# Optimization experiments

Measured on AMD Instinct MI355X. Metric: run time of the kernel, lower is better.

## Reference

```python
import jax, jax.numpy as jnp
import numpy as np

B, T, D, H = 2, 2048, 1024, 16
DK = D // H

def setup_inputs() -> dict:
    key = jax.random.key(0)
    ks = jax.random.split(key, 12)
    s = 1.0 / np.sqrt(D)
    inp = {
        'Q': jax.random.normal(ks[0], (B, T, D), jnp.float32),
        'K': jax.random.normal(ks[1], (B, T, D), jnp.float32),
        'V': jax.random.normal(ks[2], (B, T, D), jnp.float32),
        'mask': jnp.tril(jnp.ones((T, T), jnp.int32))[None, None],  # causal [1,1,T,T]
        'Wq_w': jax.random.normal(ks[3], (D, D), jnp.float32) * s,
        'Wq_b': jax.random.normal(ks[4], (D,), jnp.float32) * s,
        'Wk_w': jax.random.normal(ks[5], (D, D), jnp.float32) * s,
        'Wk_b': jax.random.normal(ks[6], (D,), jnp.float32) * s,
        'Wv_w': jax.random.normal(ks[7], (D, D), jnp.float32) * s,
        'Wv_b': jax.random.normal(ks[8], (D,), jnp.float32) * s,
        'Wo_w': jax.random.normal(ks[9], (D, D), jnp.float32) * s,
        'Wo_b': jax.random.normal(ks[10], (D,), jnp.float32) * s,
    }
    return inp

def reference(Q, K, V, mask, Wq_w, Wq_b, Wk_w, Wk_b, Wv_w, Wv_b, Wo_w, Wo_b):
    b, tq, c = Q.shape
    tk = K.shape[1]
    q = (Q @ Wq_w + Wq_b).reshape(b, tq, H, DK).transpose(0, 2, 1, 3)  # [B,H,Tq,dk]
    k = (K @ Wk_w + Wk_b).reshape(b, tk, H, DK).transpose(0, 2, 1, 3)
    v = (V @ Wv_w + Wv_b).reshape(b, tk, H, DK).transpose(0, 2, 1, 3)
    scores = jnp.einsum('bhqd,bhkd->bhqk', q, k) / jnp.sqrt(jnp.float32(DK))
    scores = jnp.where(mask == 0, jnp.float32(-1e9), scores)
    attn = jax.nn.softmax(scores, axis=-1)
    out = jnp.einsum('bhqk,bhkd->bhqd', attn, v)
    out = out.transpose(0, 2, 1, 3).reshape(b, tq, c)
    return out @ Wo_w + Wo_b
```

## Files before the change

### kernel.cpp

```cpp
#include <hip/hip_runtime.h>
#include <hip/hip_bf16.h>

#define NB 2
#define NT 2048
#define ND 1024
#define NH 16
#define NDK 64

typedef __attribute__((ext_vector_type(8))) short bf16x8;
typedef __attribute__((ext_vector_type(4))) float f32x4;

static __device__ __forceinline__ short f2bf(float f) {
  union { float f; unsigned u; } c; c.f = f;
  unsigned u = c.u;
  u += 0x7FFF + ((u >> 16) & 1);
  return (short)(u >> 16);
}

static __device__ __forceinline__ unsigned cvt_pk_bf16(float lo, float hi) {
  unsigned r;
  asm("v_cvt_pk_bf16_f32 %0, %1, %2" : "=v"(r) : "v"(lo), "v"(hi));
  return r;
}

static __device__ __forceinline__ void gload16(const void* g, void* l) {
  __builtin_amdgcn_global_load_lds((const __attribute__((address_space(1))) void*)g,
                                   (__attribute__((address_space(3))) void*)l, 16, 0, 0);
}

__global__ void cast3_kernel(const float* __restrict__ s0, const float* __restrict__ s1,
                             const float* __restrict__ s2,
                             short* __restrict__ t0, short* __restrict__ t1,
                             short* __restrict__ t2) {
  int z = blockIdx.x >> 11;
  int i = (blockIdx.x & 2047) * 256 + threadIdx.x;
  const float* src = z == 0 ? s0 : (z == 1 ? s1 : s2);
  short* dst       = z == 0 ? t0 : (z == 1 ? t1 : t2);
  const float4* s4 = (const float4*)src + (size_t)i * 2;
  float4 a = s4[0], b = s4[1];
  bf16x8 o;
  o[0] = f2bf(a.x); o[1] = f2bf(a.y); o[2] = f2bf(a.z); o[3] = f2bf(a.w);
  o[4] = f2bf(b.x); o[5] = f2bf(b.y); o[6] = f2bf(b.z); o[7] = f2bf(b.w);
  *((bf16x8*)dst + i) = o;
}

__global__ void wtrans_kernel(const float* __restrict__ W0, const float* __restrict__ W1,
                              const float* __restrict__ W2, const float* __restrict__ W3,
                              short* __restrict__ T0, short* __restrict__ T1,
                              short* __restrict__ T2, short* __restrict__ T3) {
  __shared__ float t[32][33];
  int z = blockIdx.z;
  const float* W = z == 0 ? W0 : (z == 1 ? W1 : (z == 2 ? W2 : W3));
  short* Wt      = z == 0 ? T0 : (z == 1 ? T1 : (z == 2 ? T2 : T3));
  int n0 = blockIdx.x * 32, k0 = blockIdx.y * 32;
  int tx = threadIdx.x, ty = threadIdx.y;
  for (int i = ty; i < 32; i += 8) t[i][tx] = W[(size_t)(k0 + i) * ND + n0 + tx];
  __syncthreads();
  for (int i = ty; i < 32; i += 8) Wt[(size_t)(n0 + i) * ND + k0 + tx] = f2bf(t[tx][i]);
}

template <int MODE, int BN>
__global__ __launch_bounds__(256, 2) void gemm_bt(
    const short* __restrict__ A0, const short* __restrict__ A1, const short* __restrict__ A2,
    const short* __restrict__ W0, const short* __restrict__ W1, const short* __restrict__ W2,
    const float* __restrict__ b0, const float* __restrict__ b1, const float* __restrict__ b2,
    void* o0, void* o1, void* o2)
{
  constexpr int K = ND;
  constexpr int NI = BN / 32;
  constexpr int NNB = ND / BN;
  constexpr int NZ = (MODE == 0) ? 3 : 1;
  constexpr int NWPX = NZ * 32 * NNB / 8;
  __shared__ short As[2][128 * 32];
  __shared__ short Bs[2][BN * 32];

  int d = blockIdx.x;
  int work = (d & 7) * NWPX + (d >> 3);
  int z = work / (32 * NNB);
  int rem = work % (32 * NNB);
  int m0 = (rem / NNB) * 128, n0 = (rem % NNB) * BN;

  const short* A    = z == 0 ? A0 : (z == 1 ? A1 : A2);
  const short* Wt   = z == 0 ? W0 : (z == 1 ? W1 : W2);
  const float* bias = z == 0 ? b0 : (z == 1 ? b1 : b2);
  void* out         = z == 0 ? o0 : (z == 1 ? o1 : o2);
  float scl = (MODE == 0 && z == 0) ? 0.18033688011112042f : 1.0f;

  int tid = threadIdx.x, wid = tid >> 6, lane = tid & 63;
  int wr = wid >> 1, wc = wid & 1;
  int r16 = lane & 15, l4 = lane >> 4;

  auto stage = [&](int buf, int kt) {
    int row = (lane >> 2);
    int c8 = (lane & 3) * 8;
    {
      int rbase = wid * 32;
      const short* ga = A + (size_t)(m0 + rbase + row) * K + kt * 32 + c8;
      gload16(ga,          &As[buf][rbase * 32]);
      gload16(ga + 16 * K, &As[buf][(rbase + 16) * 32]);
    }
    if constexpr (BN == 128) {
      int rbase = wid * 32;
      const short* gb = Wt + (size_t)(n0 + rbase + row) * K + kt * 32 + c8;
      gload16(gb,          &Bs[buf][rbase * 32]);
      gload16(gb + 16 * K, &Bs[buf][(rbase + 16) * 32]);
    } else {
      int rbase = wid * 16;
      const short* gb = Wt + (size_t)(n0 + rbase + row) * K + kt * 32 + c8;
      gload16(gb,          &Bs[buf][rbase * 32]);
    }
  };

  f32x4 acc[4][NI] = {};
  stage(0, 0);
  __syncthreads();

  for (int kt = 0; kt < K / 32; ++kt) {
    int cur = kt & 1;
    if (kt + 1 < K / 32) stage(cur ^ 1, kt + 1);
    bf16x8 af[4], bfv[NI];
    int kk = l4 * 8;
#pragma unroll
    for (int mi = 0; mi < 4; mi++)
      af[mi] = *(const bf16x8*)&As[cur][(wr * 64 + mi * 16 + r16) * 32 + kk];
#pragma unroll
    for (int ni = 0; ni < NI; ni++)
      bfv[ni] = *(const bf16x8*)&Bs[cur][(wc * (BN / 2) + ni * 16 + r16) * 32 + kk];
#pragma unroll
    for (int mi = 0; mi < 4; mi++)
#pragma unroll
      for (int ni = 0; ni < NI; ni++)
        acc[mi][ni] = __builtin_amdgcn_mfma_f32_16x16x32_bf16(af[mi], bfv[ni], acc[mi][ni], 0, 0, 0);
    __syncthreads();
  }

  int mb = m0 + wr * 64, nb = n0 + wc * (BN / 2);
#pragma unroll
  for (int mi = 0; mi < 4; mi++)
#pragma unroll
    for (int ni = 0; ni < NI; ni++) {
      int n = nb + ni * 16 + r16;
      float bv = bias[n];
      if constexpr (MODE == 0) {
        int h = n >> 6, dk = n & 63;
        if (z == 2) {
          int m0_ = mb + mi * 16 + l4 * 4;
          int bI = m0_ >> 11, t0 = m0_ & (NT - 1);
          int bh = bI * NH + h;
          short4 s4;
          s4.x = f2bf(acc[mi][ni][0] + bv);
          s4.y = f2bf(acc[mi][ni][1] + bv);
          s4.z = f2bf(acc[mi][ni][2] + bv);
          s4.w = f2bf(acc[mi][ni][3] + bv);
          *(short4*)&((short*)out)[(size_t)bh * 131072 + (dk >> 4) * 32768 +
                                   (t0 >> 3) * 128 + (dk & 15) * 8 + (t0 & 7)] = s4;
        } else if (z == 1) {
#pragma unroll
          for (int r = 0; r < 4; r++) {
            int m = mb + mi * 16 + l4 * 4 + r;
            int bI = m >> 11, t = m & (NT - 1);
            int bh = bI * NH + h;
            ((short*)out)[(size_t)bh * 131072 + (t >> 4) * 1024 + (dk >> 3) * 128 +
                          (t & 15) * 8 + (dk & 7)] = f2bf(acc[mi][ni][r] + bv);
          }
        } else {
#pragma unroll
          for (int r = 0; r < 4; r++) {
            int m = mb + mi * 16 + l4 * 4 + r;
            int bI = m >> 11, t = m & (NT - 1);
            ((short*)out)[((((size_t)bI * NH + h) * NT + t) << 6) + dk] = f2bf((acc[mi][ni][r] + bv) * scl);
          }
        }
      } else {
#pragma unroll
        for (int r = 0; r < 4; r++) {
          int m = mb + mi * 16 + l4 * 4 + r;
          ((float*)out)[(size_t)m * ND + n] = acc[mi][ni][r] + bv;
        }
      }
    }
}

__global__ __launch_bounds__(256) void attn_kernel(
    const short* __restrict__ q, const short* __restrict__ k, const short* __restrict__ vt,
    short* __restrict__ O)
{
  struct SH {
    union {
      short p2[4][2][16][72];
      struct {
        f32x4 obuf[4][2][2][64];
        float ol[4][32];
      } mg;
    };
  };
  __shared__ SH sh;

  int d = blockIdx.x;
  int xcd = d & 7, jj = d >> 3;
  int bh = xcd * 4 + (jj >> 6);
  int qg = 63 - (jj & 63);
  int b = bh >> 4, h = bh & 15;
  int tid = threadIdx.x, wid = tid >> 6, lane = tid & 63;
  int r16 = lane & 15, l4 = lane >> 4;
  size_t hb = (size_t)bh * NT * NDK;
  const short* qh = q + hb;
  const short* kh = k + hb;
  const short* vh = vt + hb;
  int qw = qg * 32;

  bf16x8 qa[2][2];
#pragma unroll
  for (int rf = 0; rf < 2; rf++)
#pragma unroll
    for (int kf = 0; kf < 2; kf++)
      qa[rf][kf] = *(const bf16x8*)(qh + (size_t)(qw + rf * 16 + r16) * NDK + kf * 32 + l4 * 8);

  f32x4 of[2][4] = {};
  float l_[2] = { 0.f, 0.f };

  int nt = (qw + 95) >> 6;

  bf16x8 kfr[4][2];
  if (wid < nt) {
#pragma unroll
    for (int cf = 0; cf < 4; cf++) {
      const short* kb_ = kh + (size_t)((wid * 64 >> 4) + cf) * 1024 + lane * 8;
      kfr[cf][0] = *(const bf16x8*)kb_;
      kfr[cf][1] = *(const bf16x8*)(kb_ + 512);
    }
  }

  for (int kt = wid; kt < nt; kt += 4) {
    int kv0 = kt * 64;

    f32x4 sf[2][4] = {};
    __builtin_amdgcn_s_setprio(1);
#pragma unroll
    for (int cf = 0; cf < 4; cf++) {
      sf[0][cf] = __builtin_amdgcn_mfma_f32_16x16x32_bf16(kfr[cf][0], qa[0][0], sf[0][cf], 0, 0, 0);
      sf[1][cf] = __builtin_amdgcn_mfma_f32_16x16x32_bf16(kfr[cf][0], qa[1][0], sf[1][cf], 0, 0, 0);
      sf[0][cf] = __builtin_amdgcn_mfma_f32_16x16x32_bf16(kfr[cf][1], qa[0][1], sf[0][cf], 0, 0, 0);
      sf[1][cf] = __builtin_amdgcn_mfma_f32_16x16x32_bf16(kfr[cf][1], qa[1][1], sf[1][cf], 0, 0, 0);
    }
    __builtin_amdgcn_s_setprio(0);

    {
      int ktn = (kt + 4 < nt) ? kt + 4 : kt;
      int kvn = ktn * 64;
#pragma unroll
      for (int cf = 0; cf < 4; cf++) {
        const short* kb_ = kh + (size_t)((kvn >> 4) + cf) * 1024 + lane * 8;
        kfr[cf][0] = *(const bf16x8*)kb_;
        kfr[cf][1] = *(const bf16x8*)(kb_ + 512);
      }
    }

    bf16x8 vb[4][2];
#pragma unroll
    for (int df = 0; df < 4; df++)
#pragma unroll
      for (int kf = 0; kf < 2; kf++)
        vb[df][kf] = *(const bf16x8*)(vh + df * 32768 + (kv0 >> 3) * 128 + kf * 512 + lane * 8);

    if (kv0 + 63 > qw) {
#pragma unroll
      for (int rf = 0; rf < 2; rf++)
#pragma unroll
        for (int cf = 0; cf < 4; cf++)
#pragma unroll
          for (int r = 0; r < 4; r++) {
            int kvi = kv0 + cf * 16 + l4 * 4 + r;
            int qi = qw + rf * 16 + r16;
            if (kvi > qi) sf[rf][cf][r] = -1e30f;
          }
    }

#pragma unroll
    for (int rf = 0; rf < 2; rf++) {
      float rs = 0.f;
#pragma unroll
      for (int cf = 0; cf < 4; cf++) {
        float p0 = __builtin_amdgcn_exp2f(sf[rf][cf][0]);
        float p1 = __builtin_amdgcn_exp2f(sf[rf][cf][1]);
        float p2v = __builtin_amdgcn_exp2f(sf[rf][cf][2]);
        float p3 = __builtin_amdgcn_exp2f(sf[rf][cf][3]);
        rs += (p0 + p1) + (p2v + p3);
        unsigned w0 = cvt_pk_bf16(p0, p1);
        unsigned w1 = cvt_pk_bf16(p2v, p3);
        *(int2*)&sh.p2[wid][rf][r16][cf * 16 + l4 * 4] = make_int2((int)w0, (int)w1);
      }
      l_[rf] += rs;
    }

    __builtin_amdgcn_s_setprio(1);
#pragma unroll
    for (int rf = 0; rf < 2; rf++)
#pragma unroll
      for (int kf = 0; kf < 2; kf++) {
        bf16x8 pa = *(const bf16x8*)&sh.p2[wid][rf][r16][kf * 32 + l4 * 8];
#pragma unroll
        for (int df = 0; df < 4; df++)
          of[rf][df] = __builtin_amdgcn_mfma_f32_16x16x32_bf16(vb[df][kf], pa, of[rf][df], 0, 0, 0);
      }
    __builtin_amdgcn_s_setprio(0);
  }

#pragma unroll
  for (int rf = 0; rf < 2; rf++) {
    float t = l_[rf];
    t += __shfl_xor(t, 16);
    t += __shfl_xor(t, 32);
    l_[rf] = t;
  }

  __syncthreads();
  if (l4 == 0) {
    sh.mg.ol[wid][r16] = l_[0];
    sh.mg.ol[wid][16 + r16] = l_[1];
  }
#pragma unroll
  for (int pass = 0; pass < 2; ++pass) {
#pragma unroll
    for (int rf = 0; rf < 2; rf++)
#pragma unroll
      for (int dfp = 0; dfp < 2; dfp++)
        sh.mg.obuf[wid][rf][dfp][lane] = of[rf][2 * pass + dfp];
    __syncthreads();
    {
      int mrf = wid >> 1, mdfp = wid & 1, mdf = 2 * pass + mdfp;
      int row = mrf * 16 + r16;
      float lst = sh.mg.ol[0][row] + sh.mg.ol[1][row] + sh.mg.ol[2][row] + sh.mg.ol[3][row];
      float rinv = 1.0f / lst;
      f32x4 o0 = sh.mg.obuf[0][mrf][mdfp][lane];
      f32x4 o1 = sh.mg.obuf[1][mrf][mdfp][lane];
      f32x4 o2 = sh.mg.obuf[2][mrf][mdfp][lane];
      f32x4 o3 = sh.mg.obuf[3][mrf][mdfp][lane];
      float v0 = (o0[0] + o1[0] + o2[0] + o3[0]) * rinv;
      float v1 = (o0[1] + o1[1] + o2[1] + o3[1]) * rinv;
      float v2 = (o0[2] + o1[2] + o2[2] + o3[2]) * rinv;
      float v3 = (o0[3] + o1[3] + o2[3] + o3[3]) * rinv;
      int t = qw + mrf * 16 + r16;
      *(int2*)&O[(size_t)(b * NT + t) * ND + h * 64 + mdf * 16 + l4 * 4] =
          make_int2((int)cvt_pk_bf16(v0, v1), (int)cvt_pk_bf16(v2, v3));
    }
    __syncthreads();
  }
}

extern "C" void kernel_launch(void* const* d_in, const int* in_sizes, int n_in,
                              void* d_out, int out_size, void* d_ws, size_t ws_size,
                              hipStream_t stream)
{
  const float* Q  = (const float*)d_in[0];
  const float* Ki = (const float*)d_in[1];
  const float* V  = (const float*)d_in[2];
  const float* Wq = (const float*)d_in[4];  const float* bq = (const float*)d_in[5];
  const float* Wk = (const float*)d_in[6];  const float* bk = (const float*)d_in[7];
  const float* Wv = (const float*)d_in[8];  const float* bv = (const float*)d_in[9];
  const float* Wo = (const float*)d_in[10]; const float* bo = (const float*)d_in[11];

  short* ws = (short*)d_ws;
  const size_t M4 = (size_t)4 * 1024 * 1024;
  short* Qb  = ws;
  short* Kb  = ws + M4;
  short* Vb  = ws + 2 * M4;
  short* qp  = ws + 3 * M4;
  short* kp  = ws + 4 * M4;
  short* vtp = ws + 5 * M4;
  short* Wqt = ws + 6 * M4;
  short* Wkt = Wqt + 1024 * 1024;
  short* Wvt = Wkt + 1024 * 1024;
  short* Wot = Wvt + 1024 * 1024;
  short* Obuf = Qb;

  cast3_kernel<<<6144, 256, 0, stream>>>(Q, Ki, V, Qb, Kb, Vb);
  wtrans_kernel<<<dim3(32, 32, 4), dim3(32, 8), 0, stream>>>(Wq, Wk, Wv, Wo,
                                                             Wqt, Wkt, Wvt, Wot);

  gemm_bt<0, 128><<<768, 256, 0, stream>>>(Qb, Kb, Vb, Wqt, Wkt, Wvt,
                                           bq, bk, bv, qp, kp, vtp);
  attn_kernel<<<2048, 256, 0, stream>>>(qp, kp, vtp, Obuf);
  gemm_bt<1, 64><<<512, 256, 0, stream>>>(Obuf, Obuf, Obuf, Wot, Wot, Wot,
                                          bo, bo, bo, d_out, d_out, d_out);
}
```

Baseline: 120.3 us.

## Merge prep kernels into one launch and split attention rows into staggered halves

Fuses the input cast and weight transpose kernels into a single prep launch, removing one kernel launch and its tail. In the attention inner loop, the score MFMAs are split into two row-fragment groups and the softmax plus PV MFMAs for the first half are issued before the second half's exp work. This lets matrix and vector ALU work interleave. The s_setprio hints are removed. The change adds more sequential dependencies per half and alters register live ranges.

After: 115.8 us. -3.8%, faster.

```diff
diff --git a/kernel.cpp b/kernel.cpp
--- a/kernel.cpp
+++ b/kernel.cpp
@@ -28,35 +28,38 @@
                                    (__attribute__((address_space(3))) void*)l, 16, 0, 0);
 }
 
-__global__ void cast3_kernel(const float* __restrict__ s0, const float* __restrict__ s1,
-                             const float* __restrict__ s2,
-                             short* __restrict__ t0, short* __restrict__ t1,
-                             short* __restrict__ t2) {
-  int z = blockIdx.x >> 11;
-  int i = (blockIdx.x & 2047) * 256 + threadIdx.x;
-  const float* src = z == 0 ? s0 : (z == 1 ? s1 : s2);
-  short* dst       = z == 0 ? t0 : (z == 1 ? t1 : t2);
-  const float4* s4 = (const float4*)src + (size_t)i * 2;
-  float4 a = s4[0], b = s4[1];
-  bf16x8 o;
-  o[0] = f2bf(a.x); o[1] = f2bf(a.y); o[2] = f2bf(a.z); o[3] = f2bf(a.w);
-  o[4] = f2bf(b.x); o[5] = f2bf(b.y); o[6] = f2bf(b.z); o[7] = f2bf(b.w);
-  *((bf16x8*)dst + i) = o;
-}
-
-__global__ void wtrans_kernel(const float* __restrict__ W0, const float* __restrict__ W1,
-                              const float* __restrict__ W2, const float* __restrict__ W3,
-                              short* __restrict__ T0, short* __restrict__ T1,
-                              short* __restrict__ T2, short* __restrict__ T3) {
+__global__ void prep_kernel(const float* __restrict__ Q, const float* __restrict__ Ki,
+                            const float* __restrict__ V,
+                            short* __restrict__ Qb, short* __restrict__ Kb, short* __restrict__ Vb,
+                            const float* __restrict__ W0, const float* __restrict__ W1,
+                            const float* __restrict__ W2, const float* __restrict__ W3,
+                            short* __restrict__ T0, short* __restrict__ T1,
+                            short* __restrict__ T2, short* __restrict__ T3) {
   __shared__ float t[32][33];
-  int z = blockIdx.z;
-  const float* W = z == 0 ? W0 : (z == 1 ? W1 : (z == 2 ? W2 : W3));
-  short* Wt      = z == 0 ? T0 : (z == 1 ? T1 : (z == 2 ? T2 : T3));
-  int n0 = blockIdx.x * 32, k0 = blockIdx.y * 32;
-  int tx = threadIdx.x, ty = threadIdx.y;
-  for (int i = ty; i < 32; i += 8) t[i][tx] = W[(size_t)(k0 + i) * ND + n0 + tx];
-  __syncthreads();
-  for (int i = ty; i < 32; i += 8) Wt[(size_t)(n0 + i) * ND + k0 + tx] = f2bf(t[tx][i]);
+  int d = blockIdx.x, tid = threadIdx.x;
+  if (d < 6144) {
+    int z = d >> 11;
+    int i = (d & 2047) * 256 + tid;
+    const float* src = z == 0 ? Q : (z == 1 ? Ki : V);
+    short* dst       = z == 0 ? Qb : (z == 1 ? Kb : Vb);
+    const float4* s4 = (const float4*)src + (size_t)i * 2;
+    float4 a = s4[0], b = s4[1];
+    bf16x8 o;
+    o[0] = f2bf(a.x); o[1] = f2bf(a.y); o[2] = f2bf(a.z); o[3] = f2bf(a.w);
+    o[4] = f2bf(b.x); o[5] = f2bf(b.y); o[6] = f2bf(b.z); o[7] = f2bf(b.w);
+    *((bf16x8*)dst + i) = o;
+  } else {
+    int dd = d - 6144;
+    int z = dd >> 10;
+    int rem = dd & 1023;
+    const float* W = z == 0 ? W0 : (z == 1 ? W1 : (z == 2 ? W2 : W3));
+    short* Wt      = z == 0 ? T0 : (z == 1 ? T1 : (z == 2 ? T2 : T3));
+    int n0 = (rem & 31) * 32, k0 = (rem >> 5) * 32;
+    int tx = tid & 31, ty = tid >> 5;
+    for (int i = ty; i < 32; i += 8) t[i][tx] = W[(size_t)(k0 + i) * ND + n0 + tx];
+    __syncthreads();
+    for (int i = ty; i < 32; i += 8) Wt[(size_t)(n0 + i) * ND + k0 + tx] = f2bf(t[tx][i]);
+  }
 }
 
 template <int MODE, int BN>
@@ -217,7 +220,7 @@
       qa[rf][kf] = *(const bf16x8*)(qh + (size_t)(qw + rf * 16 + r16) * NDK + kf * 32 + l4 * 8);
 
   f32x4 of[2][4] = {};
-  float l_[2] = { 0.f, 0.f };
+  float l0 = 0.f, l1 = 0.f;
 
   int nt = (qw + 95) >> 6;
 
@@ -233,17 +236,18 @@
 
   for (int kt = wid; kt < nt; kt += 4) {
     int kv0 = kt * 64;
-
     f32x4 sf[2][4] = {};
-    __builtin_amdgcn_s_setprio(1);
+
 #pragma unroll
     for (int cf = 0; cf < 4; cf++) {
       sf[0][cf] = __builtin_amdgcn_mfma_f32_16x16x32_bf16(kfr[cf][0], qa[0][0], sf[0][cf], 0, 0, 0);
+      sf[0][cf] = __builtin_amdgcn_mfma_f32_16x16x32_bf16(kfr[cf][1], qa[0][1], sf[0][cf], 0, 0, 0);
+    }
+#pragma unroll
+    for (int cf = 0; cf < 4; cf++) {
       sf[1][cf] = __builtin_amdgcn_mfma_f32_16x16x32_bf16(kfr[cf][0], qa[1][0], sf[1][cf], 0, 0, 0);
-      sf[0][cf] = __builtin_amdgcn_mfma_f32_16x16x32_bf16(kfr[cf][1], qa[0][1], sf[0][cf], 0, 0, 0);
       sf[1][cf] = __builtin_amdgcn_mfma_f32_16x16x32_bf16(kfr[cf][1], qa[1][1], sf[1][cf], 0, 0, 0);
     }
-    __builtin_amdgcn_s_setprio(0);
 
     {
       int ktn = (kt + 4 < nt) ? kt + 4 : kt;
@@ -263,61 +267,80 @@
       for (int kf = 0; kf < 2; kf++)
         vb[df][kf] = *(const bf16x8*)(vh + df * 32768 + (kv0 >> 3) * 128 + kf * 512 + lane * 8);
 
-    if (kv0 + 63 > qw) {
-#pragma unroll
-      for (int rf = 0; rf < 2; rf++)
-#pragma unroll
-        for (int cf = 0; cf < 4; cf++)
-#pragma unroll
-          for (int r = 0; r < 4; r++) {
-            int kvi = kv0 + cf * 16 + l4 * 4 + r;
-            int qi = qw + rf * 16 + r16;
-            if (kvi > qi) sf[rf][cf][r] = -1e30f;
-          }
-    }
-
-#pragma unroll
-    for (int rf = 0; rf < 2; rf++) {
+    bool nm = (kv0 + 63 > qw);
+
+    if (nm) {
+#pragma unroll
+      for (int cf = 0; cf < 4; cf++)
+#pragma unroll
+        for (int r = 0; r < 4; r++) {
+          int kvi = kv0 + cf * 16 + l4 * 4 + r;
+          if (kvi > qw + r16) sf[0][cf][r] = -1e30f;
+        }
+    }
+    {
       float rs = 0.f;
 #pragma unroll
       for (int cf = 0; cf < 4; cf++) {
-        float p0 = __builtin_amdgcn_exp2f(sf[rf][cf][0]);
-        float p1 = __builtin_amdgcn_exp2f(sf[rf][cf][1]);
-        float p2v = __builtin_amdgcn_exp2f(sf[rf][cf][2]);
-        float p3 = __builtin_amdgcn_exp2f(sf[rf][cf][3]);
+        float p0 = __builtin_amdgcn_exp2f(sf[0][cf][0]);
+        float p1 = __builtin_amdgcn_exp2f(sf[0][cf][1]);
+        float p2v = __builtin_amdgcn_exp2f(sf[0][cf][2]);
+        float p3 = __builtin_amdgcn_exp2f(sf[0][cf][3]);
         rs += (p0 + p1) + (p2v + p3);
         unsigned w0 = cvt_pk_bf16(p0, p1);
         unsigned w1 = cvt_pk_bf16(p2v, p3);
-        *(int2*)&sh.p2[wid][rf][r16][cf * 16 + l4 * 4] = make_int2((int)w0, (int)w1);
+        *(int2*)&sh.p2[wid][0][r16][cf * 16 + l4 * 4] = make_int2((int)w0, (int)w1);
       }
-      l_[rf] += rs;
-    }
-
-    __builtin_amdgcn_s_setprio(1);
-#pragma unroll
-    for (int rf = 0; rf < 2; rf++)
-#pragma unroll
-      for (int kf = 0; kf < 2; kf++) {
-        bf16x8 pa = *(const bf16x8*)&sh.p2[wid][rf][r16][kf * 32 + l4 * 8];
-#pragma unroll
-        for (int df = 0; df < 4; df++)
-          of[rf][df] = __builtin_amdgcn_mfma_f32_16x16x32_bf16(vb[df][kf], pa, of[rf][df], 0, 0, 0);
+      l0 += rs;
+    }
+#pragma unroll
+    for (int kf = 0; kf < 2; kf++) {
+      bf16x8 pa = *(const bf16x8*)&sh.p2[wid][0][r16][kf * 32 + l4 * 8];
+#pragma unroll
+      for (int df = 0; df < 4; df++)
+        of[0][df] = __builtin_amdgcn_mfma_f32_16x16x32_bf16(vb[df][kf], pa, of[0][df], 0, 0, 0);
+    }
+
+    if (nm) {
+#pragma unroll
+      for (int cf = 0; cf < 4; cf++)
+#pragma unroll
+        for (int r = 0; r < 4; r++) {
+          int kvi = kv0 + cf * 16 + l4 * 4 + r;
+          if (kvi > qw + 16 + r16) sf[1][cf][r] = -1e30f;
+        }
+    }
+    {
+      float rs = 0.f;
+#pragma unroll
+      for (int cf = 0; cf < 4; cf++) {
+        float p0 = __builtin_amdgcn_exp2f(sf[1][cf][0]);
+        float p1 = __builtin_amdgcn_exp2f(sf[1][cf][1]);
+        float p2v = __builtin_amdgcn_exp2f(sf[1][cf][2]);
+        float p3 = __builtin_amdgcn_exp2f(sf[1][cf][3]);
+        rs += (p0 + p1) + (p2v + p3);
+        unsigned w0 = cvt_pk_bf16(p0, p1);
+        unsigned w1 = cvt_pk_bf16(p2v, p3);
+        *(int2*)&sh.p2[wid][1][r16][cf * 16 + l4 * 4] = make_int2((int)w0, (int)w1);
       }
-    __builtin_amdgcn_s_setprio(0);
-  }
-
-#pragma unroll
-  for (int rf = 0; rf < 2; rf++) {
-    float t = l_[rf];
-    t += __shfl_xor(t, 16);
-    t += __shfl_xor(t, 32);
-    l_[rf] = t;
-  }
+      l1 += rs;
+    }
+#pragma unroll
+    for (int kf = 0; kf < 2; kf++) {
+      bf16x8 pa = *(const bf16x8*)&sh.p2[wid][1][r16][kf * 32 + l4 * 8];
+#pragma unroll
+      for (int df = 0; df < 4; df++)
+        of[1][df] = __builtin_amdgcn_mfma_f32_16x16x32_bf16(vb[df][kf], pa, of[1][df], 0, 0, 0);
+    }
+  }
+
+  l0 += __shfl_xor(l0, 16); l0 += __shfl_xor(l0, 32);
+  l1 += __shfl_xor(l1, 16); l1 += __shfl_xor(l1, 32);
 
   __syncthreads();
   if (l4 == 0) {
-    sh.mg.ol[wid][r16] = l_[0];
-    sh.mg.ol[wid][16 + r16] = l_[1];
+    sh.mg.ol[wid][r16] = l0;
+    sh.mg.ol[wid][16 + r16] = l1;
   }
 #pragma unroll
   for (int pass = 0; pass < 2; ++pass) {
@@ -374,9 +397,8 @@
   short* Wot = Wvt + 1024 * 1024;
   short* Obuf = Qb;
 
-  cast3_kernel<<<6144, 256, 0, stream>>>(Q, Ki, V, Qb, Kb, Vb);
-  wtrans_kernel<<<dim3(32, 32, 4), dim3(32, 8), 0, stream>>>(Wq, Wk, Wv, Wo,
-                                                             Wqt, Wkt, Wvt, Wot);
+  prep_kernel<<<10240, 256, 0, stream>>>(Q, Ki, V, Qb, Kb, Vb,
+                                         Wq, Wk, Wv, Wo, Wqt, Wkt, Wvt, Wot);
 
   gemm_bt<0, 128><<<768, 256, 0, stream>>>(Qb, Kb, Vb, Wqt, Wkt, Wvt,
                                            bq, bk, bv, qp, kp, vtp);
```
